# Kernel optimization log

Measured on AMD Instinct MI355X. Metric: run time of the kernel, lower is better.

## Reference

```python
import jax, jax.numpy as jnp
import numpy as np
import math

B, S, E, H = 4, 2048, 1024, 16

def setup_inputs() -> dict:
    key = jax.random.key(0)
    k1, k2, k3 = jax.random.split(key, 3)
    scale_in = 1.0 / math.sqrt(E)
    x = jax.random.normal(k1, (B, S, E), dtype=jnp.float32)
    W_attn = jax.random.normal(k2, (E, 3 * E), dtype=jnp.float32) * scale_in
    b_attn = jnp.zeros((3 * E,), dtype=jnp.float32)
    W_proj = jax.random.normal(k3, (E, E), dtype=jnp.float32) * scale_in
    b_proj = jnp.zeros((E,), dtype=jnp.float32)
    return {"x": x, "W_attn": W_attn, "b_attn": b_attn, "W_proj": W_proj, "b_proj": b_proj}

def reference(x, W_attn, b_attn, W_proj, b_proj):
    batch, seq, emb = x.shape
    hd = emb // H  # head_dim
    qkv = x @ W_attn + b_attn                      # [B,S,3E]
    q, k, v = jnp.split(qkv, 3, axis=-1)
    # [B,S,E] -> [B,H,S,hd]
    q = q.reshape(batch, seq, H, hd).transpose(0, 2, 1, 3)
    k = k.reshape(batch, seq, H, hd).transpose(0, 2, 1, 3)
    v = v.reshape(batch, seq, H, hd).transpose(0, 2, 1, 3)
    scores = jnp.einsum('bhqd,bhkd->bhqk', q, k) * (1.0 / math.sqrt(hd))
    causal = jnp.tril(jnp.ones((seq, seq), dtype=bool))
    scores = jnp.where(causal[None, None, :, :], scores, jnp.finfo(scores.dtype).min)
    attn = jax.nn.softmax(scores, axis=-1)         # dropout p=0 -> identity
    out = jnp.einsum('bhqk,bhkd->bhqd', attn, v)   # [B,H,S,hd]
    out = out.transpose(0, 2, 1, 3).reshape(batch, seq, emb)
    return out @ W_proj + b_proj
```

## Files before the change

kernel.cpp:

```cpp
#include <hip/hip_runtime.h>

typedef __bf16 bf16;
typedef __bf16 bf16x8_t __attribute__((ext_vector_type(8)));
typedef __bf16 bf16x4_t __attribute__((ext_vector_type(4)));
typedef float f32x4_t __attribute__((ext_vector_type(4)));

#define S_ 2048
#define E_ 1024
#define HD 64
#define LOG2E 1.4426950408889634f
#define QSCALE (0.125f * LOG2E)

__device__ __forceinline__ void gl_lds16(const bf16* g, bf16* l) {
  __builtin_amdgcn_global_load_lds(
      (const __attribute__((address_space(1))) unsigned int*)g,
      (__attribute__((address_space(3))) unsigned int*)l, 16, 0, 0);
}

__global__ void cvt4(const float* __restrict__ in, bf16* __restrict__ out) {
  int i = (blockIdx.x * 256 + threadIdx.x) * 4;
  float4 v = *(const float4*)(in + i);
  bf16x4_t o = { (bf16)v.x, (bf16)v.y, (bf16)v.z, (bf16)v.w };
  *(bf16x4_t*)(out + i) = o;
}

__global__ void transpose_cvt(const float* __restrict__ in, bf16* __restrict__ out,
                              int R, int C) {
  __shared__ float tile[32][33];
  int c0 = blockIdx.x * 32, r0 = blockIdx.y * 32;
  int tx = threadIdx.x & 31, ty = threadIdx.x >> 5;
#pragma unroll
  for (int i = 0; i < 32; i += 8)
    tile[ty + i][tx] = in[(size_t)(r0 + ty + i) * C + c0 + tx];
  __syncthreads();
#pragma unroll
  for (int i = 0; i < 32; i += 8)
    out[(size_t)(c0 + ty + i) * R + r0 + tx] = (bf16)tile[tx][ty + i];
}

template <int MODE>
__global__ __launch_bounds__(256, 2)
void gemm128(const bf16* __restrict__ A, const bf16* __restrict__ Bt,
             const float* __restrict__ bias,
             bf16* __restrict__ Q, bf16* __restrict__ K, bf16* __restrict__ Vt,
             float* __restrict__ Out) {
  __shared__ __align__(16) bf16 As[128 * 64];
  __shared__ __align__(16) bf16 Bs[128 * 64];
  const int tid = threadIdx.x;
  const int wave = tid >> 6, lane = tid & 63;
  const int quad = lane >> 4, l16 = lane & 15;
  const int wm = wave >> 1, wn = wave & 1;
  const int bm = blockIdx.x, bn = blockIdx.y;

  f32x4_t acc[4][4];
#pragma unroll
  for (int i = 0; i < 4; i++)
#pragma unroll
    for (int j = 0; j < 4; j++) acc[i][j] = (f32x4_t){0.f, 0.f, 0.f, 0.f};

  for (int k0 = 0; k0 < 1024; k0 += 64) {
    __syncthreads();
#pragma unroll
    for (int it = 0; it < 4; it++) {
      int id = it * 256 + tid;
      int row = id >> 3, c = id & 7;
      int sc = (c ^ (row & 7)) * 8;
      gl_lds16(A + (size_t)(bm * 128 + row) * 1024 + k0 + sc, As + id * 8);
      gl_lds16(Bt + (size_t)(bn * 128 + row) * 1024 + k0 + sc, Bs + id * 8);
    }
    __syncthreads();
#pragma unroll
    for (int ks = 0; ks < 2; ks++) {
      bf16x8_t af[4], bfr[4];
#pragma unroll
      for (int i = 0; i < 4; i++) {
        int row = wm * 64 + i * 16 + l16;
        af[i] = *(const bf16x8_t*)&As[row * 64 + (((ks * 4 + quad) ^ (row & 7)) * 8)];
      }
#pragma unroll
      for (int j = 0; j < 4; j++) {
        int row = wn * 64 + j * 16 + l16;
        bfr[j] = *(const bf16x8_t*)&Bs[row * 64 + (((ks * 4 + quad) ^ (row & 7)) * 8)];
      }
#pragma unroll
      for (int i = 0; i < 4; i++)
#pragma unroll
        for (int j = 0; j < 4; j++)
          acc[i][j] = __builtin_amdgcn_mfma_f32_16x16x32_bf16(af[i], bfr[j], acc[i][j], 0, 0, 0);
    }
  }

  if (MODE == 0) {
#pragma unroll
    for (int j = 0; j < 4; j++) {
      int n_g = bn * 128 + wn * 64 + j * 16 + l16;
      float bv = bias[n_g];
      int which = n_g >> 10;
      int cc = n_g & 1023;
      int hh = cc >> 6, dd = cc & 63;
#pragma unroll
      for (int i = 0; i < 4; i++) {
        int m0 = bm * 128 + wm * 64 + i * 16 + quad * 4;
        int bb = m0 >> 11, ss0 = m0 & 2047;
        int bhn = bb * 16 + hh;
        if (which == 2) {
          bf16x4_t pk;
#pragma unroll
          for (int r = 0; r < 4; r++) pk[r] = (bf16)(acc[i][j][r] + bv);
          *(bf16x4_t*)&Vt[((size_t)bhn * 64 + dd) * 2048 + ss0] = pk;
        } else {
          bf16* dst = (which == 0) ? Q : K;
          float scl = (which == 0) ? QSCALE : 1.f;
#pragma unroll
          for (int r = 0; r < 4; r++)
            dst[((size_t)bhn * 2048 + ss0 + r) * 64 + dd] = (bf16)((acc[i][j][r] + bv) * scl);
        }
      }
    }
  } else {
#pragma unroll
    for (int j = 0; j < 4; j++) {
      int n_g = bn * 128 + wn * 64 + j * 16 + l16;
      float bv = bias[n_g];
#pragma unroll
      for (int i = 0; i < 4; i++) {
        int m0 = bm * 128 + wm * 64 + i * 16 + quad * 4;
#pragma unroll
        for (int r = 0; r < 4; r++)
          Out[(size_t)(m0 + r) * 1024 + n_g] = acc[i][j][r] + bv;
      }
    }
  }
}

__global__ __launch_bounds__(256, 2)
void attn_kernel(const bf16* __restrict__ Q, const bf16* __restrict__ K,
                 const bf16* __restrict__ Vt, bf16* __restrict__ O) {
  __shared__ __align__(16) bf16 Ks[128 * 64];
  __shared__ __align__(16) bf16 Vs[64 * 128];
  __shared__ __align__(16) bf16 Ps[4 * 32 * 128];
  const int tid = threadIdx.x;
  const int wave = tid >> 6, lane = tid & 63;
  const int quad = lane >> 4, l16 = lane & 15;
  const int pid = blockIdx.x, bh = blockIdx.y;
  const int b = bh >> 4, h = bh & 15;

  const bf16* Qg = Q + (size_t)bh * S_ * HD;
  const bf16* Kg = K + (size_t)bh * S_ * HD;
  const bf16* Vg = Vt + (size_t)bh * HD * S_;
  bf16* Pw = Ps + wave * 4096;

  for (int qi = 0; qi < 2; qi++) {
    const int qb = qi ? (15 - pid) : pid;
    bf16x8_t qf[2][2];
#pragma unroll
    for (int ni = 0; ni < 2; ni++)
#pragma unroll
      for (int ks = 0; ks < 2; ks++)
        qf[ni][ks] = *(const bf16x8_t*)(Qg +
            (size_t)(qb * 128 + wave * 32 + ni * 16 + l16) * HD + ks * 32 + quad * 8);

    f32x4_t o[4][2];
#pragma unroll
    for (int mi = 0; mi < 4; mi++)
#pragma unroll
      for (int ni = 0; ni < 2; ni++) o[mi][ni] = (f32x4_t){0.f, 0.f, 0.f, 0.f};
    float m_[2] = {-1e30f, -1e30f}, l_[2] = {0.f, 0.f};

    for (int kb = 0; kb <= qb; kb++) {
      __syncthreads();
      const bf16* Ksrc = Kg + (size_t)kb * 128 * HD;
#pragma unroll
      for (int it = 0; it < 4; it++) {
        int id = it * 256 + tid;
        {
          int row = id >> 3, c = id & 7;
          gl_lds16(Ksrc + row * 64 + ((c ^ (row & 7)) * 8), Ks + id * 8);
        }
        {
          int d = id >> 4, c = id & 15;
          gl_lds16(Vg + (size_t)d * S_ + kb * 128 + ((c ^ (d & 7)) * 8), Vs + id * 8);
        }
      }
      __syncthreads();

      f32x4_t sacc[8][2];
#pragma unroll
      for (int mi = 0; mi < 8; mi++)
#pragma unroll
        for (int ni = 0; ni < 2; ni++) sacc[mi][ni] = (f32x4_t){0.f, 0.f, 0.f, 0.f};
#pragma unroll
      for (int ks = 0; ks < 2; ks++)
#pragma unroll
        for (int mi = 0; mi < 8; mi++) {
          int kr = mi * 16 + l16;
          bf16x8_t kf = *(const bf16x8_t*)&Ks[kr * 64 + (((ks * 4 + quad) ^ (kr & 7)) * 8)];
          sacc[mi][0] = __builtin_amdgcn_mfma_f32_16x16x32_bf16(kf, qf[0][ks], sacc[mi][0], 0, 0, 0);
          sacc[mi][1] = __builtin_amdgcn_mfma_f32_16x16x32_bf16(kf, qf[1][ks], sacc[mi][1], 0, 0, 0);
        }

      if (kb == qb) {
#pragma unroll
        for (int mi = 0; mi < 8; mi++)
#pragma unroll
          for (int ni = 0; ni < 2; ni++) {
            int qrow = wave * 32 + ni * 16 + l16;
            int krow = mi * 16 + quad * 4;
#pragma unroll
            for (int r = 0; r < 4; r++)
              if (krow + r > qrow) sacc[mi][ni][r] = -1e30f;
          }
      }

#pragma unroll
      for (int ni = 0; ni < 2; ni++) {
        float mx = sacc[0][ni][0];
#pragma unroll
        for (int mi = 0; mi < 8; mi++)
#pragma unroll
          for (int r = 0; r < 4; r++) mx = fmaxf(mx, sacc[mi][ni][r]);
        mx = fmaxf(mx, __shfl_xor(mx, 16));
        mx = fmaxf(mx, __shfl_xor(mx, 32));
        float mnew = fmaxf(m_[ni], mx);
        float alpha = __builtin_amdgcn_exp2f(m_[ni] - mnew);
        m_[ni] = mnew;
        float rs = 0.f;
#pragma unroll
        for (int mi = 0; mi < 8; mi++)
#pragma unroll
          for (int r = 0; r < 4; r++) {
            float p = __builtin_amdgcn_exp2f(sacc[mi][ni][r] - mnew);
            sacc[mi][ni][r] = p;
            rs += p;
          }
        rs += __shfl_xor(rs, 16);
        rs += __shfl_xor(rs, 32);
        l_[ni] = alpha * l_[ni] + rs;
#pragma unroll
        for (int mi = 0; mi < 4; mi++)
#pragma unroll
          for (int r = 0; r < 4; r++) o[mi][ni][r] *= alpha;
      }

#pragma unroll
      for (int ni = 0; ni < 2; ni++) {
        int qr = ni * 16 + l16;
#pragma unroll
        for (int mi = 0; mi < 8; mi++) {
          bf16x4_t pk;
#pragma unroll
          for (int r = 0; r < 4; r++) pk[r] = (bf16)sacc[mi][ni][r];
          int c = mi * 2 + (quad >> 1);
          *(bf16x4_t*)&Pw[qr * 128 + ((c ^ (qr & 7)) * 8) + (quad & 1) * 4] = pk;
        }
      }

#pragma unroll
      for (int ks2 = 0; ks2 < 4; ks2++) {
        bf16x8_t vb[4], pa[2];
#pragma unroll
        for (int mi = 0; mi < 4; mi++) {
          int d = mi * 16 + l16;
          vb[mi] = *(const bf16x8_t*)&Vs[d * 128 + (((ks2 * 4 + quad) ^ (d & 7)) * 8)];
        }
#pragma unroll
        for (int ni = 0; ni < 2; ni++) {
          int qr = ni * 16 + l16;
          pa[ni] = *(const bf16x8_t*)&Pw[qr * 128 + (((ks2 * 4 + quad) ^ (qr & 7)) * 8)];
        }
#pragma unroll
        for (int mi = 0; mi < 4; mi++)
#pragma unroll
          for (int ni = 0; ni < 2; ni++)
            o[mi][ni] = __builtin_amdgcn_mfma_f32_16x16x32_bf16(vb[mi], pa[ni], o[mi][ni], 0, 0, 0);
      }
    }

#pragma unroll
    for (int ni = 0; ni < 2; ni++) {
      float inv = 1.0f / l_[ni];
      int q_g = qb * 128 + wave * 32 + ni * 16 + l16;
      size_t rowb = (size_t)(b * S_ + q_g) * E_ + h * HD;
#pragma unroll
      for (int mi = 0; mi < 4; mi++) {
        bf16x4_t ov;
#pragma unroll
        for (int r = 0; r < 4; r++) ov[r] = (bf16)(o[mi][ni][r] * inv);
        *(bf16x4_t*)&O[rowb + mi * 16 + quad * 4] = ov;
      }
    }
  }
}

extern "C" void kernel_launch(void* const* d_in, const int* in_sizes, int n_in,
                              void* d_out, int out_size, void* d_ws, size_t ws_size,
                              hipStream_t stream) {
  const float* x      = (const float*)d_in[0];
  const float* W_attn = (const float*)d_in[1];
  const float* b_attn = (const float*)d_in[2];
  const float* W_proj = (const float*)d_in[3];
  const float* b_proj = (const float*)d_in[4];
  float* out = (float*)d_out;

  bf16* xb  = (bf16*)d_ws;
  bf16* Wat = xb + 8388608ull;
  bf16* Wpt = Wat + 3145728ull;
  bf16* Qb  = Wpt + 1048576ull;
  bf16* Kb  = Qb + 8388608ull;
  bf16* Vtb = Kb + 8388608ull;
  bf16* AOb = xb;

  cvt4<<<8192, 256, 0, stream>>>(x, xb);
  transpose_cvt<<<dim3(96, 32), 256, 0, stream>>>(W_attn, Wat, 1024, 3072);
  transpose_cvt<<<dim3(32, 32), 256, 0, stream>>>(W_proj, Wpt, 1024, 1024);
  gemm128<0><<<dim3(64, 24), 256, 0, stream>>>(xb, Wat, b_attn, Qb, Kb, Vtb, nullptr);
  attn_kernel<<<dim3(8, 64), 256, 0, stream>>>(Qb, Kb, Vtb, AOb);
  gemm128<1><<<dim3(64, 8), 256, 0, stream>>>(AOb, Wpt, b_proj, nullptr, nullptr, nullptr, out);
}
```

Baseline: 247.4 us.

## Double-buffer K/V tiles in attention and halve the per-wave P buffer

The attention kernel now prefetches the next K and V tile into a second LDS buffer with async global-to-LDS loads while the current tile is being computed. This removes the load-then-barrier stall at the start of each key-block iteration, and it also prefetches the first tile of the second query block. To pay for the extra LDS, the P staging buffer is halved: the PV product runs in two 64-column halves that reuse the same per-wave space. Total dynamic LDS grows to 80 KB per block, which only keeps two blocks per CU if the device has 160 KB of LDS. Correctness depends on the barrier waiting for the outstanding async loads.

New measurement: 248.1 us. No clear change (+0.3%).

```diff
diff --git a/kernel.cpp b/kernel.cpp
--- a/kernel.cpp
+++ b/kernel.cpp
@@ -136,9 +136,10 @@
 __global__ __launch_bounds__(256, 2)
 void attn_kernel(const bf16* __restrict__ Q, const bf16* __restrict__ K,
                  const bf16* __restrict__ Vt, bf16* __restrict__ O) {
-  __shared__ __align__(16) bf16 Ks[128 * 64];
-  __shared__ __align__(16) bf16 Vs[64 * 128];
-  __shared__ __align__(16) bf16 Ps[4 * 32 * 128];
+  extern __shared__ __align__(16) bf16 smem[];
+  bf16* Ks = smem;
+  bf16* Vs = smem + 16384;
+  bf16* Ps = smem + 32768;
   const int tid = threadIdx.x;
   const int wave = tid >> 6, lane = tid & 63;
   const int quad = lane >> 4, l16 = lane & 15;
@@ -148,7 +149,29 @@
   const bf16* Qg = Q + (size_t)bh * S_ * HD;
   const bf16* Kg = K + (size_t)bh * S_ * HD;
   const bf16* Vg = Vt + (size_t)bh * HD * S_;
-  bf16* Pw = Ps + wave * 4096;
+  bf16* Pw = Ps + wave * 2048;
+
+  auto stage = [&](int c, int kb) {
+    const bf16* Ksrc = Kg + (size_t)kb * 128 * HD;
+    const bf16* Vsrc = Vg + kb * 128;
+    bf16* Kd = Ks + c * 8192;
+    bf16* Vd = Vs + c * 8192;
+#pragma unroll
+    for (int it = 0; it < 4; it++) {
+      int id = it * 256 + tid;
+      {
+        int row = id >> 3, cc = id & 7;
+        gl_lds16(Ksrc + row * 64 + ((cc ^ (row & 7)) * 8), Kd + id * 8);
+      }
+      {
+        int d = id >> 4, cc = id & 15;
+        gl_lds16(Vsrc + (size_t)d * S_ + ((cc ^ (d & 7)) * 8), Vd + id * 8);
+      }
+    }
+  };
+
+  int cur = 0;
+  stage(0, 0);
 
   for (int qi = 0; qi < 2; qi++) {
     const int qb = qi ? (15 - pid) : pid;
@@ -167,22 +190,14 @@
       for (int ni = 0; ni < 2; ni++) o[mi][ni] = (f32x4_t){0.f, 0.f, 0.f, 0.f};
     float m_[2] = {-1e30f, -1e30f}, l_[2] = {0.f, 0.f};
 
+    if (qi == 0) __syncthreads();
+
     for (int kb = 0; kb <= qb; kb++) {
-      __syncthreads();
-      const bf16* Ksrc = Kg + (size_t)kb * 128 * HD;
-#pragma unroll
-      for (int it = 0; it < 4; it++) {
-        int id = it * 256 + tid;
-        {
-          int row = id >> 3, c = id & 7;
-          gl_lds16(Ksrc + row * 64 + ((c ^ (row & 7)) * 8), Ks + id * 8);
-        }
-        {
-          int d = id >> 4, c = id & 15;
-          gl_lds16(Vg + (size_t)d * S_ + kb * 128 + ((c ^ (d & 7)) * 8), Vs + id * 8);
-        }
-      }
-      __syncthreads();
+      if (kb < qb) stage(cur ^ 1, kb + 1);
+      else if (qi == 0) stage(cur ^ 1, 0);
+
+      const bf16* Kc = Ks + cur * 8192;
+      const bf16* Vc = Vs + cur * 8192;
 
       f32x4_t sacc[8][2];
 #pragma unroll
@@ -194,7 +209,7 @@
 #pragma unroll
         for (int mi = 0; mi < 8; mi++) {
           int kr = mi * 16 + l16;
-          bf16x8_t kf = *(const bf16x8_t*)&Ks[kr * 64 + (((ks * 4 + quad) ^ (kr & 7)) * 8)];
+          bf16x8_t kf = *(const bf16x8_t*)&Kc[kr * 64 + (((ks * 4 + quad) ^ (kr & 7)) * 8)];
           sacc[mi][0] = __builtin_amdgcn_mfma_f32_16x16x32_bf16(kf, qf[0][ks], sacc[mi][0], 0, 0, 0);
           sacc[mi][1] = __builtin_amdgcn_mfma_f32_16x16x32_bf16(kf, qf[1][ks], sacc[mi][1], 0, 0, 0);
         }
@@ -243,37 +258,43 @@
       }
 
 #pragma unroll
-      for (int ni = 0; ni < 2; ni++) {
-        int qr = ni * 16 + l16;
-#pragma unroll
-        for (int mi = 0; mi < 8; mi++) {
-          bf16x4_t pk;
-#pragma unroll
-          for (int r = 0; r < 4; r++) pk[r] = (bf16)sacc[mi][ni][r];
-          int c = mi * 2 + (quad >> 1);
-          *(bf16x4_t*)&Pw[qr * 128 + ((c ^ (qr & 7)) * 8) + (quad & 1) * 4] = pk;
-        }
-      }
-
-#pragma unroll
-      for (int ks2 = 0; ks2 < 4; ks2++) {
-        bf16x8_t vb[4], pa[2];
-#pragma unroll
-        for (int mi = 0; mi < 4; mi++) {
-          int d = mi * 16 + l16;
-          vb[mi] = *(const bf16x8_t*)&Vs[d * 128 + (((ks2 * 4 + quad) ^ (d & 7)) * 8)];
-        }
+      for (int hh = 0; hh < 2; hh++) {
 #pragma unroll
         for (int ni = 0; ni < 2; ni++) {
           int qr = ni * 16 + l16;
-          pa[ni] = *(const bf16x8_t*)&Pw[qr * 128 + (((ks2 * 4 + quad) ^ (qr & 7)) * 8)];
+#pragma unroll
+          for (int mm = 0; mm < 4; mm++) {
+            bf16x4_t pk;
+#pragma unroll
+            for (int r = 0; r < 4; r++) pk[r] = (bf16)sacc[hh * 4 + mm][ni][r];
+            int c = mm * 2 + (quad >> 1);
+            *(bf16x4_t*)&Pw[qr * 64 + ((c ^ (qr & 7)) * 8) + (quad & 1) * 4] = pk;
+          }
         }
 #pragma unroll
-        for (int mi = 0; mi < 4; mi++)
-#pragma unroll
-          for (int ni = 0; ni < 2; ni++)
-            o[mi][ni] = __builtin_amdgcn_mfma_f32_16x16x32_bf16(vb[mi], pa[ni], o[mi][ni], 0, 0, 0);
-      }
+        for (int k2 = 0; k2 < 2; k2++) {
+          int ks2 = hh * 2 + k2;
+          bf16x8_t vb[4], pa[2];
+#pragma unroll
+          for (int mi = 0; mi < 4; mi++) {
+            int d = mi * 16 + l16;
+            vb[mi] = *(const bf16x8_t*)&Vc[d * 128 + (((ks2 * 4 + quad) ^ (d & 7)) * 8)];
+          }
+#pragma unroll
+          for (int ni = 0; ni < 2; ni++) {
+            int qr = ni * 16 + l16;
+            pa[ni] = *(const bf16x8_t*)&Pw[qr * 64 + (((k2 * 4 + quad) ^ (qr & 7)) * 8)];
+          }
+#pragma unroll
+          for (int mi = 0; mi < 4; mi++)
+#pragma unroll
+            for (int ni = 0; ni < 2; ni++)
+              o[mi][ni] = __builtin_amdgcn_mfma_f32_16x16x32_bf16(vb[mi], pa[ni], o[mi][ni], 0, 0, 0);
+        }
+      }
+
+      __syncthreads();
+      cur ^= 1;
     }
 
 #pragma unroll
@@ -314,6 +335,6 @@
   transpose_cvt<<<dim3(96, 32), 256, 0, stream>>>(W_attn, Wat, 1024, 3072);
   transpose_cvt<<<dim3(32, 32), 256, 0, stream>>>(W_proj, Wpt, 1024, 1024);
   gemm128<0><<<dim3(64, 24), 256, 0, stream>>>(xb, Wat, b_attn, Qb, Kb, Vtb, nullptr);
-  attn_kernel<<<dim3(8, 64), 256, 0, stream>>>(Qb, Kb, Vtb, AOb);
+  attn_kernel<<<dim3(8, 64), 256, 81920, stream>>>(Qb, Kb, Vtb, AOb);
   gemm128<1><<<dim3(64, 8), 256, 0, stream>>>(AOb, Wpt, b_proj, nullptr, nullptr, nullptr, out);
 }
```

## Cut attention LDS by reusing K buffer for P, raise occupancy, one q-block per CTA

Applied to the files above, without the earlier changes.

The separate per-wave P scratch buffer is removed, and P is written in two halves into the K tile region after an extra barrier. This cuts LDS per block from 64KB to 32KB so launch bounds can be raised to 4 blocks per CU. The paired causal q-block loop is replaced by one q-block per CTA over a doubled grid. The change also tree-reduces the row max and sum, and raises wave priority around the MFMA sections. The costs are an extra __syncthreads per key block, tighter register limits and possible spills, and the loss of the triangular load balancing the paired blocks gave.

New measurement: 406.9 us. 64.5% more time.

```diff
diff --git a/kernel.cpp b/kernel.cpp
--- a/kernel.cpp
+++ b/kernel.cpp
@@ -15,6 +15,13 @@
   __builtin_amdgcn_global_load_lds(
       (const __attribute__((address_space(1))) unsigned int*)g,
       (__attribute__((address_space(3))) unsigned int*)l, 16, 0, 0);
+}
+
+__device__ __forceinline__ f32x4_t vmax4(f32x4_t a, f32x4_t b) {
+  f32x4_t r;
+  r[0] = fmaxf(a[0], b[0]); r[1] = fmaxf(a[1], b[1]);
+  r[2] = fmaxf(a[2], b[2]); r[3] = fmaxf(a[3], b[3]);
+  return r;
 }
 
 __global__ void cvt4(const float* __restrict__ in, bf16* __restrict__ out) {
@@ -133,130 +140,138 @@
   }
 }
 
-__global__ __launch_bounds__(256, 2)
+__global__ __launch_bounds__(256, 4)
 void attn_kernel(const bf16* __restrict__ Q, const bf16* __restrict__ K,
                  const bf16* __restrict__ Vt, bf16* __restrict__ O) {
   __shared__ __align__(16) bf16 Ks[128 * 64];
   __shared__ __align__(16) bf16 Vs[64 * 128];
-  __shared__ __align__(16) bf16 Ps[4 * 32 * 128];
   const int tid = threadIdx.x;
   const int wave = tid >> 6, lane = tid & 63;
   const int quad = lane >> 4, l16 = lane & 15;
-  const int pid = blockIdx.x, bh = blockIdx.y;
+  const int qb = blockIdx.x, bh = blockIdx.y;
   const int b = bh >> 4, h = bh & 15;
 
   const bf16* Qg = Q + (size_t)bh * S_ * HD;
   const bf16* Kg = K + (size_t)bh * S_ * HD;
   const bf16* Vg = Vt + (size_t)bh * HD * S_;
-  bf16* Pw = Ps + wave * 4096;
-
-  for (int qi = 0; qi < 2; qi++) {
-    const int qb = qi ? (15 - pid) : pid;
-    bf16x8_t qf[2][2];
-#pragma unroll
-    for (int ni = 0; ni < 2; ni++)
-#pragma unroll
-      for (int ks = 0; ks < 2; ks++)
-        qf[ni][ks] = *(const bf16x8_t*)(Qg +
-            (size_t)(qb * 128 + wave * 32 + ni * 16 + l16) * HD + ks * 32 + quad * 8);
-
-    f32x4_t o[4][2];
-#pragma unroll
-    for (int mi = 0; mi < 4; mi++)
-#pragma unroll
-      for (int ni = 0; ni < 2; ni++) o[mi][ni] = (f32x4_t){0.f, 0.f, 0.f, 0.f};
-    float m_[2] = {-1e30f, -1e30f}, l_[2] = {0.f, 0.f};
-
-    for (int kb = 0; kb <= qb; kb++) {
-      __syncthreads();
-      const bf16* Ksrc = Kg + (size_t)kb * 128 * HD;
-#pragma unroll
-      for (int it = 0; it < 4; it++) {
-        int id = it * 256 + tid;
-        {
-          int row = id >> 3, c = id & 7;
-          gl_lds16(Ksrc + row * 64 + ((c ^ (row & 7)) * 8), Ks + id * 8);
-        }
-        {
-          int d = id >> 4, c = id & 15;
-          gl_lds16(Vg + (size_t)d * S_ + kb * 128 + ((c ^ (d & 7)) * 8), Vs + id * 8);
-        }
-      }
-      __syncthreads();
-
-      f32x4_t sacc[8][2];
+  bf16* Pw = Ks + wave * 2048;
+
+  bf16x8_t qf[2][2];
+#pragma unroll
+  for (int ni = 0; ni < 2; ni++)
+#pragma unroll
+    for (int ks = 0; ks < 2; ks++)
+      qf[ni][ks] = *(const bf16x8_t*)(Qg +
+          (size_t)(qb * 128 + wave * 32 + ni * 16 + l16) * HD + ks * 32 + quad * 8);
+
+  f32x4_t o[4][2];
+#pragma unroll
+  for (int mi = 0; mi < 4; mi++)
+#pragma unroll
+    for (int ni = 0; ni < 2; ni++) o[mi][ni] = (f32x4_t){0.f, 0.f, 0.f, 0.f};
+  float m_[2] = {-1e30f, -1e30f}, l_[2] = {0.f, 0.f};
+
+  for (int kb = 0; kb <= qb; kb++) {
+    __syncthreads();
+#pragma unroll
+    for (int it = 0; it < 4; it++) {
+      int id = it * 256 + tid;
+      {
+        int row = id >> 3, cc = id & 7;
+        gl_lds16(Kg + (size_t)kb * 128 * HD + row * 64 + ((cc ^ (row & 7)) * 8),
+                 Ks + id * 8);
+      }
+      {
+        int d = id >> 4, cc = id & 15;
+        gl_lds16(Vg + (size_t)d * S_ + kb * 128 + ((cc ^ (d & 7)) * 8), Vs + id * 8);
+      }
+    }
+    __syncthreads();
+
+    f32x4_t sacc[8][2];
+#pragma unroll
+    for (int mi = 0; mi < 8; mi++)
+#pragma unroll
+      for (int ni = 0; ni < 2; ni++) sacc[mi][ni] = (f32x4_t){0.f, 0.f, 0.f, 0.f};
+    __builtin_amdgcn_s_setprio(1);
+#pragma unroll
+    for (int ks = 0; ks < 2; ks++)
+#pragma unroll
+      for (int mi = 0; mi < 8; mi++) {
+        int kr = mi * 16 + l16;
+        bf16x8_t kf = *(const bf16x8_t*)&Ks[kr * 64 + (((ks * 4 + quad) ^ (kr & 7)) * 8)];
+        sacc[mi][0] = __builtin_amdgcn_mfma_f32_16x16x32_bf16(kf, qf[0][ks], sacc[mi][0], 0, 0, 0);
+        sacc[mi][1] = __builtin_amdgcn_mfma_f32_16x16x32_bf16(kf, qf[1][ks], sacc[mi][1], 0, 0, 0);
+      }
+    __builtin_amdgcn_s_setprio(0);
+
+    if (kb == qb) {
 #pragma unroll
       for (int mi = 0; mi < 8; mi++)
 #pragma unroll
-        for (int ni = 0; ni < 2; ni++) sacc[mi][ni] = (f32x4_t){0.f, 0.f, 0.f, 0.f};
-#pragma unroll
-      for (int ks = 0; ks < 2; ks++)
-#pragma unroll
-        for (int mi = 0; mi < 8; mi++) {
-          int kr = mi * 16 + l16;
-          bf16x8_t kf = *(const bf16x8_t*)&Ks[kr * 64 + (((ks * 4 + quad) ^ (kr & 7)) * 8)];
-          sacc[mi][0] = __builtin_amdgcn_mfma_f32_16x16x32_bf16(kf, qf[0][ks], sacc[mi][0], 0, 0, 0);
-          sacc[mi][1] = __builtin_amdgcn_mfma_f32_16x16x32_bf16(kf, qf[1][ks], sacc[mi][1], 0, 0, 0);
-        }
-
-      if (kb == qb) {
-#pragma unroll
-        for (int mi = 0; mi < 8; mi++)
-#pragma unroll
-          for (int ni = 0; ni < 2; ni++) {
-            int qrow = wave * 32 + ni * 16 + l16;
-            int krow = mi * 16 + quad * 4;
-#pragma unroll
-            for (int r = 0; r < 4; r++)
-              if (krow + r > qrow) sacc[mi][ni][r] = -1e30f;
-          }
-      }
-
-#pragma unroll
-      for (int ni = 0; ni < 2; ni++) {
-        float mx = sacc[0][ni][0];
-#pragma unroll
-        for (int mi = 0; mi < 8; mi++)
-#pragma unroll
-          for (int r = 0; r < 4; r++) mx = fmaxf(mx, sacc[mi][ni][r]);
-        mx = fmaxf(mx, __shfl_xor(mx, 16));
-        mx = fmaxf(mx, __shfl_xor(mx, 32));
-        float mnew = fmaxf(m_[ni], mx);
-        float alpha = __builtin_amdgcn_exp2f(m_[ni] - mnew);
-        m_[ni] = mnew;
-        float rs = 0.f;
-#pragma unroll
-        for (int mi = 0; mi < 8; mi++)
-#pragma unroll
-          for (int r = 0; r < 4; r++) {
-            float p = __builtin_amdgcn_exp2f(sacc[mi][ni][r] - mnew);
-            sacc[mi][ni][r] = p;
-            rs += p;
-          }
-        rs += __shfl_xor(rs, 16);
-        rs += __shfl_xor(rs, 32);
-        l_[ni] = alpha * l_[ni] + rs;
-#pragma unroll
-        for (int mi = 0; mi < 4; mi++)
-#pragma unroll
-          for (int r = 0; r < 4; r++) o[mi][ni][r] *= alpha;
-      }
-
+        for (int ni = 0; ni < 2; ni++) {
+          int qrow = wave * 32 + ni * 16 + l16;
+          int krow = mi * 16 + quad * 4;
+#pragma unroll
+          for (int r = 0; r < 4; r++)
+            if (krow + r > qrow) sacc[mi][ni][r] = -1e30f;
+        }
+    }
+
+#pragma unroll
+    for (int ni = 0; ni < 2; ni++) {
+      f32x4_t t0 = vmax4(sacc[0][ni], sacc[1][ni]);
+      f32x4_t t1 = vmax4(sacc[2][ni], sacc[3][ni]);
+      f32x4_t t2 = vmax4(sacc[4][ni], sacc[5][ni]);
+      f32x4_t t3 = vmax4(sacc[6][ni], sacc[7][ni]);
+      t0 = vmax4(t0, t1); t2 = vmax4(t2, t3); t0 = vmax4(t0, t2);
+      float mx = fmaxf(fmaxf(t0[0], t0[1]), fmaxf(t0[2], t0[3]));
+      mx = fmaxf(mx, __shfl_xor(mx, 16));
+      mx = fmaxf(mx, __shfl_xor(mx, 32));
+      float mnew = fmaxf(m_[ni], mx);
+      float alpha = __builtin_amdgcn_exp2f(m_[ni] - mnew);
+      m_[ni] = mnew;
+      f32x4_t a0 = {0.f, 0.f, 0.f, 0.f}, a1 = {0.f, 0.f, 0.f, 0.f};
+#pragma unroll
+      for (int mi = 0; mi < 4; mi++) {
+#pragma unroll
+        for (int r = 0; r < 4; r++) {
+          sacc[mi][ni][r] = __builtin_amdgcn_exp2f(sacc[mi][ni][r] - mnew);
+          sacc[mi + 4][ni][r] = __builtin_amdgcn_exp2f(sacc[mi + 4][ni][r] - mnew);
+        }
+        a0 += sacc[mi][ni];
+        a1 += sacc[mi + 4][ni];
+      }
+      a0 += a1;
+      float rs = (a0[0] + a0[1]) + (a0[2] + a0[3]);
+      rs += __shfl_xor(rs, 16);
+      rs += __shfl_xor(rs, 32);
+      l_[ni] = alpha * l_[ni] + rs;
+#pragma unroll
+      for (int mi = 0; mi < 4; mi++)
+#pragma unroll
+        for (int r = 0; r < 4; r++) o[mi][ni][r] *= alpha;
+    }
+
+    __syncthreads();
+
+#pragma unroll
+    for (int hh = 0; hh < 2; hh++) {
 #pragma unroll
       for (int ni = 0; ni < 2; ni++) {
         int qr = ni * 16 + l16;
 #pragma unroll
-        for (int mi = 0; mi < 8; mi++) {
+        for (int mm = 0; mm < 4; mm++) {
           bf16x4_t pk;
 #pragma unroll
-          for (int r = 0; r < 4; r++) pk[r] = (bf16)sacc[mi][ni][r];
-          int c = mi * 2 + (quad >> 1);
-          *(bf16x4_t*)&Pw[qr * 128 + ((c ^ (qr & 7)) * 8) + (quad & 1) * 4] = pk;
-        }
-      }
-
-#pragma unroll
-      for (int ks2 = 0; ks2 < 4; ks2++) {
+          for (int r = 0; r < 4; r++) pk[r] = (bf16)sacc[hh * 4 + mm][ni][r];
+          int c = mm * 2 + (quad >> 1);
+          *(bf16x4_t*)&Pw[qr * 64 + ((c ^ (qr & 7)) * 8) + (quad & 1) * 4] = pk;
+        }
+      }
+#pragma unroll
+      for (int k2 = 0; k2 < 2; k2++) {
+        int ks2 = hh * 2 + k2;
         bf16x8_t vb[4], pa[2];
 #pragma unroll
         for (int mi = 0; mi < 4; mi++) {
@@ -266,28 +281,30 @@
 #pragma unroll
         for (int ni = 0; ni < 2; ni++) {
           int qr = ni * 16 + l16;
-          pa[ni] = *(const bf16x8_t*)&Pw[qr * 128 + (((ks2 * 4 + quad) ^ (qr & 7)) * 8)];
-        }
+          pa[ni] = *(const bf16x8_t*)&Pw[qr * 64 + (((k2 * 4 + quad) ^ (qr & 7)) * 8)];
+        }
+        __builtin_amdgcn_s_setprio(1);
 #pragma unroll
         for (int mi = 0; mi < 4; mi++)
 #pragma unroll
           for (int ni = 0; ni < 2; ni++)
             o[mi][ni] = __builtin_amdgcn_mfma_f32_16x16x32_bf16(vb[mi], pa[ni], o[mi][ni], 0, 0, 0);
-      }
-    }
-
-#pragma unroll
-    for (int ni = 0; ni < 2; ni++) {
-      float inv = 1.0f / l_[ni];
-      int q_g = qb * 128 + wave * 32 + ni * 16 + l16;
-      size_t rowb = (size_t)(b * S_ + q_g) * E_ + h * HD;
-#pragma unroll
-      for (int mi = 0; mi < 4; mi++) {
-        bf16x4_t ov;
-#pragma unroll
-        for (int r = 0; r < 4; r++) ov[r] = (bf16)(o[mi][ni][r] * inv);
-        *(bf16x4_t*)&O[rowb + mi * 16 + quad * 4] = ov;
-      }
+        __builtin_amdgcn_s_setprio(0);
+      }
+    }
+  }
+
+#pragma unroll
+  for (int ni = 0; ni < 2; ni++) {
+    float inv = 1.0f / l_[ni];
+    int q_g = qb * 128 + wave * 32 + ni * 16 + l16;
+    size_t rowb = (size_t)(b * S_ + q_g) * E_ + h * HD;
+#pragma unroll
+    for (int mi = 0; mi < 4; mi++) {
+      bf16x4_t ov;
+#pragma unroll
+      for (int r = 0; r < 4; r++) ov[r] = (bf16)(o[mi][ni][r] * inv);
+      *(bf16x4_t*)&O[rowb + mi * 16 + quad * 4] = ov;
     }
   }
 }
@@ -314,6 +331,6 @@
   transpose_cvt<<<dim3(96, 32), 256, 0, stream>>>(W_attn, Wat, 1024, 3072);
   transpose_cvt<<<dim3(32, 32), 256, 0, stream>>>(W_proj, Wpt, 1024, 1024);
   gemm128<0><<<dim3(64, 24), 256, 0, stream>>>(xb, Wat, b_attn, Qb, Kb, Vtb, nullptr);
-  attn_kernel<<<dim3(8, 64), 256, 0, stream>>>(Qb, Kb, Vtb, AOb);
+  attn_kernel<<<dim3(16, 64), 256, 0, stream>>>(Qb, Kb, Vtb, AOb);
   gemm128<1><<<dim3(64, 8), 256, 0, stream>>>(AOb, Wpt, b_proj, nullptr, nullptr, nullptr, out);
 }
```
